# Performance work log

Measured on AMD Instinct MI355X. Metric: run time of the kernel, lower is better.

Reference implementation:

```python
import jax, jax.numpy as jnp
import numpy as np

B, S, D, NH = 8, 2048, 1024, 8
HD = D // NH          # 128 head dim
UP = 2752             # round_up(2.6667*1024, 64) gated FFN up dim
EPS = 1e-6


def setup_inputs() -> dict:
    key = jax.random.key(0)
    ks = jax.random.split(key, 10)
    s_hd = 1.0 / np.sqrt(HD)
    s_d = 1.0 / np.sqrt(D)
    s_up = 1.0 / np.sqrt(UP)
    return {
        "x": jax.random.normal(ks[0], (B, S, D), jnp.float32),
        "rms1_w": 1.0 + 0.1 * jax.random.normal(ks[1], (D,), jnp.float32),
        "rms2_w": 1.0 + 0.1 * jax.random.normal(ks[2], (D,), jnp.float32),
        # block-diagonal per-head input projections for the 4 gates (i,f,z,o)
        "Wg": jax.random.normal(ks[3], (4, NH, HD, HD), jnp.float32) * s_hd,
        # block-diagonal per-head recurrent weights for the 4 gates
        "R": jax.random.normal(ks[4], (4, NH, HD, HD), jnp.float32) * s_hd,
        "b": jax.random.normal(ks[5], (4, D), jnp.float32) * 0.1,
        "gn_w": 1.0 + 0.1 * jax.random.normal(ks[6], (D,), jnp.float32),
        "W_gate": jax.random.normal(ks[7], (D, UP), jnp.float32) * s_d,
        "W_up": jax.random.normal(ks[8], (D, UP), jnp.float32) * s_d,
        "W_down": jax.random.normal(ks[9], (UP, D), jnp.float32) * s_up,
    }


def _rmsnorm(x, w):
    xf = x.astype(jnp.float32)
    return xf * jax.lax.rsqrt(jnp.mean(xf * xf, axis=-1, keepdims=True) + EPS) * w


def _slstm_block(x, rms1_w, rms2_w, Wg, R, b, gn_w, W_gate, W_up, W_down):
    # --- norm + sLSTM layer ---
    xn = _rmsnorm(x, rms1_w)                     # [B,S,D]
    xh = xn.reshape(B, S, NH, HD)
    # precompute input-side gate preactivations for all timesteps: [S,B,4,NH,HD]
    gx = jnp.einsum('bsni,gnoi->sbgno', xh, Wg) + b.reshape(4, NH, HD)

    zeros = jnp.zeros((B, NH, HD), jnp.float32)
    init = (zeros, zeros, zeros, zeros)          # h, c, n, m

    def step(carry, g):
        h, c, n, m = carry
        pre = g + jnp.einsum('bni,gnoi->bgno', h, R)   # [B,4,NH,HD]
        ir, fr, zr, o_r = pre[:, 0], pre[:, 1], pre[:, 2], pre[:, 3]
        logfplusm = m + jax.nn.log_sigmoid(fr)
        mnew = jnp.maximum(ir, logfplusm)
        i = jnp.exp(ir - mnew)
        f = jnp.exp(logfplusm - mnew)
        cnew = f * c + i * jnp.tanh(zr)
        nnew = f * n + i
        hnew = jax.nn.sigmoid(o_r) * cnew / nnew
        return (hnew, cnew, nnew, mnew), hnew

    (hl, cl, nl, ml), hs = jax.lax.scan(step, init, gx)
    hs = jnp.transpose(hs, (1, 0, 2, 3))         # [B,S,NH,HD]
    # per-head group norm (zero-mean layernorm within each head), weight only
    mu = jnp.mean(hs, axis=-1, keepdims=True)
    var = jnp.var(hs, axis=-1, keepdims=True)
    y = ((hs - mu) * jax.lax.rsqrt(var + EPS)).reshape(B, S, D) * gn_w
    x = x + y                                    # residual
    # --- norm + gated SiLU FFN ---
    xn2 = _rmsnorm(x, rms2_w)
    ff = (jax.nn.silu(xn2 @ W_gate) * (xn2 @ W_up)) @ W_down
    out = x + ff
    state = jnp.stack([hl, cl, nl, ml])          # [4,B,NH,HD] last (h,c,n,m)
    return out, state


def reference(x, rms1_w, rms2_w, Wg, R, b, gn_w, W_gate, W_up, W_down):
    return _slstm_block(x, rms1_w, rms2_w, Wg, R, b, gn_w, W_gate, W_up, W_down)
```

## Files before the change

kernel.cpp:

```cpp
#include <hip/hip_runtime.h>

typedef __bf16 bf16;
typedef bf16 bf16x8 __attribute__((ext_vector_type(8)));
typedef bf16 bf16x4 __attribute__((ext_vector_type(4)));
typedef float f32x4 __attribute__((ext_vector_type(4)));

#define B_ 8
#define S_ 2048
#define D_ 1024
#define NH_ 8
#define HD_ 128
#define UPP 2816
#define ROWS (B_*S_)

__device__ __forceinline__ void gload_lds16(const void* gsrc, void* ldsdst) {
  __builtin_amdgcn_global_load_lds(
      (const __attribute__((address_space(1))) void*)gsrc,
      (__attribute__((address_space(3))) void*)ldsdst, 16, 0, 0);
}

__global__ __launch_bounds__(256) void pack_wgr_kernel(
    const float* __restrict__ Wg, const float* __restrict__ R, const float* __restrict__ bv,
    bf16* __restrict__ Wgpk, bf16* __restrict__ Rpk, float* __restrict__ biaspk)
{
  const float K2 = 1.442695040888963f;
  int idx = blockIdx.x * 256 + threadIdx.x;
  if (idx < 8*512*128) {
    int k = idx & 127, j = (idx >> 7) & 511, n = idx >> 16;
    int g = (j >> 4) & 3, o = ((j >> 6) << 4) | (j & 15);
    float sc = (g == 2) ? 2.f*K2 : K2;
    size_t src = (((size_t)(g*8 + n)*128 + o)*128 + k);
    Wgpk[idx] = (bf16)(Wg[src] * sc);
    Rpk[idx]  = (bf16)(R[src] * sc);
  }
  if (idx < 8*512) {
    int j = idx & 511, n = idx >> 9;
    int g = (j >> 4) & 3, o = ((j >> 6) << 4) | (j & 15);
    float sc = (g == 2) ? 2.f*K2 : K2;
    biaspk[idx] = bv[g*1024 + n*128 + o] * sc;
  }
}

__global__ __launch_bounds__(256) void packT_kernel(
    const float* __restrict__ in, bf16* __restrict__ out,
    int K_out, int N_out, int K_in, int N_in)
{
  __shared__ float tile[64][65];
  int k0 = blockIdx.x * 64, j0 = blockIdx.y * 64;
  int tj = threadIdx.x & 63, t4 = threadIdx.x >> 6;
  #pragma unroll
  for (int p = 0; p < 16; ++p) {
    int kk = p*4 + t4, k = k0 + kk, j = j0 + tj;
    tile[kk][tj] = (k < K_in && j < N_in) ? in[(size_t)k * N_in + j] : 0.f;
  }
  __syncthreads();
  #pragma unroll
  for (int p = 0; p < 16; ++p) {
    int jj = p*4 + t4, j = j0 + jj, k = k0 + tj;
    if (j < N_out && k < K_out) out[(size_t)j * K_out + k] = (bf16)tile[tj][jj];
  }
}

__global__ __launch_bounds__(256) void rmsnorm1_kernel(
    const float* __restrict__ x, const float* __restrict__ w, bf16* __restrict__ xn)
{
  const int row = blockIdx.x, t = threadIdx.x;
  const size_t base = (size_t)row * D_;
  float4 xv = ((const float4*)(x + base))[t];
  float p = xv.x*xv.x + xv.y*xv.y + xv.z*xv.z + xv.w*xv.w;
  #pragma unroll
  for (int m = 1; m <= 32; m <<= 1) p += __shfl_xor(p, m);
  __shared__ float red[4];
  if ((t & 63) == 0) red[t >> 6] = p;
  __syncthreads();
  float rs = rsqrtf((red[0]+red[1]+red[2]+red[3]) * (1.f/1024.f) + 1e-6f);
  float4 wv = ((const float4*)w)[t];
  bf16x4 o;
  o[0] = (bf16)(xv.x*rs*wv.x); o[1] = (bf16)(xv.y*rs*wv.y);
  o[2] = (bf16)(xv.z*rs*wv.z); o[3] = (bf16)(xv.w*rs*wv.w);
  ((bf16x4*)(xn + base))[t] = o;
}

#define BM 128
#define BN 128
#define BKK 64
template<int MODE>
__global__ __launch_bounds__(256) void gemm_bt(
    const bf16* __restrict__ A, int lda,
    const bf16* __restrict__ B, int ldb,
    float* Cf, bf16* Cb, int ldc,
    const float* __restrict__ bias, const float* res, const bf16* gatein, int K)
{
  __shared__ __align__(16) bf16 As[BM*BKK];
  __shared__ __align__(16) bf16 Bs[BN*BKK];
  if constexpr (MODE == 0) {
    const int h = blockIdx.z;
    A += h * HD_;
    B += (size_t)h * (512*128);
    Cb += (size_t)h * ((size_t)ROWS * 512);
    bias += h * 512;
  }
  const int tid = threadIdx.x;
  const int lane = tid & 63, wave = tid >> 6;
  const int row0 = blockIdx.y * BM, col0 = blockIdx.x * BN;
  const int srow = lane >> 3, scol = (lane & 7) * 8;
  const int wr = (wave >> 1) * 64, wc = (wave & 1) * 64;
  const int fr = lane & 15, fg = lane >> 4;
  f32x4 acc[4][4] = {};

  for (int k0 = 0; k0 < K; k0 += BKK) {
    __syncthreads();
    #pragma unroll
    for (int c = 0; c < 4; ++c) {
      const int slot = wave * 4 + c;
      const int r = slot * 8 + srow;
      gload_lds16(A + (size_t)(row0 + r) * lda + (k0 + scol), &As[slot * 512]);
      gload_lds16(B + (size_t)(col0 + r) * ldb + (k0 + scol), &Bs[slot * 512]);
    }
    __syncthreads();
    #pragma unroll
    for (int kk = 0; kk < 2; ++kk) {
      bf16x8 af[4], bfv[4];
      #pragma unroll
      for (int m = 0; m < 4; ++m)
        af[m] = *(const bf16x8*)&As[(wr + m*16 + fr)*BKK + kk*32 + fg*8];
      #pragma unroll
      for (int nn = 0; nn < 4; ++nn)
        bfv[nn] = *(const bf16x8*)&Bs[(wc + nn*16 + fr)*BKK + kk*32 + fg*8];
      #pragma unroll
      for (int m = 0; m < 4; ++m)
        #pragma unroll
        for (int nn = 0; nn < 4; ++nn)
          acc[m][nn] = __builtin_amdgcn_mfma_f32_16x16x32_bf16(af[m], bfv[nn], acc[m][nn], 0, 0, 0);
    }
  }

  #pragma unroll
  for (int m = 0; m < 4; ++m) {
    const int rbase = row0 + wr + m*16 + fg*4;
    #pragma unroll
    for (int nn = 0; nn < 4; ++nn) {
      const int col = col0 + wc + nn*16 + fr;
      #pragma unroll
      for (int j = 0; j < 4; ++j) {
        const size_t off = (size_t)(rbase + j) * ldc + col;
        float v = acc[m][nn][j];
        if constexpr (MODE == 0) Cb[off] = (bf16)(v + bias[col]);
        if constexpr (MODE == 1) Cb[off] = (bf16)v;
        if constexpr (MODE == 2) Cf[off] = v + res[off];
        if constexpr (MODE == 3) {
          float gf = (float)gatein[off];
          Cb[off] = (bf16)(gf / (1.f + __expf(-gf)) * v);
        }
      }
    }
  }
}

__global__ __launch_bounds__(256, 1) void recur_kernel(
    const bf16* __restrict__ gx, const bf16* __restrict__ Rpk,
    bf16* __restrict__ hs, float* __restrict__ stateOut)
{
  const int n = blockIdx.x;
  const int tid = threadIdx.x, w = tid >> 6, l = tid & 63;
  const int b16 = l & 15, fg = l >> 4;
  const int b8 = l & 7, q8 = (l >> 3) & 1;
  __shared__ __align__(16) bf16 H0[16*136];
  __shared__ __align__(16) bf16 H1[16*136];
  for (int i = tid; i < 16*136; i += 256) { H0[i] = (bf16)0.f; H1[i] = (bf16)0.f; }
  __syncthreads();

  bf16x8 rf[8][4];
  #pragma unroll
  for (int tt = 0; tt < 8; ++tt)
    #pragma unroll
    for (int kk = 0; kk < 4; ++kk)
      rf[tt][kk] = *(const bf16x8*)&Rpk[(size_t)n*65536 + (size_t)(w*128 + tt*16 + b16)*128 + kk*32 + fg*8];

  f32x4 zv = {0.f, 0.f, 0.f, 0.f};
  asm volatile("" : "+v"(zv));

  float cS[4] = {}, nS[4] = {}, mS[4] = {}, hv[4] = {};
  const int o0 = w*32 + q8*16 + fg*4;
  const bf16* gxp = gx + (size_t)n * ROWS * 512 + (size_t)b8 * S_ * 512
                    + (size_t)(2*w + q8) * 64 + fg*4;
  bf16* hsp = hs + (size_t)b8 * S_ * D_ + n * HD_ + o0;

  bf16x4 gb0[4], gb1[4], gb2[4], gb3[4];
  #pragma unroll
  for (int g = 0; g < 4; ++g) {
    gb0[g] = *(const bf16x4*)(gxp + (size_t)0*512 + g*16);
    gb1[g] = *(const bf16x4*)(gxp + (size_t)1*512 + g*16);
  }

  auto step = [&](bf16* Hr, bf16* Hw, int s, bf16x4 (&gU)[4], bf16x4 (&gF)[4]) {
    bf16x8 hf[4];
    #pragma unroll
    for (int kk = 0; kk < 4; ++kk)
      hf[kk] = *(const bf16x8*)&Hr[b16*136 + kk*32 + fg*8];

    {
      int sf = (s + 2 < S_) ? s + 2 : 0;
      #pragma unroll
      for (int g = 0; g < 4; ++g)
        gF[g] = *(const bf16x4*)(gxp + (size_t)sf*512 + g*16);
    }

    f32x4 acc[8];
    #pragma unroll
    for (int tt = 0; tt < 8; ++tt)
      acc[tt] = __builtin_amdgcn_mfma_f32_16x16x32_bf16(rf[tt][0], hf[0], zv, 0, 0, 0);
    #pragma unroll
    for (int kk = 1; kk < 4; ++kk)
      #pragma unroll
      for (int tt = 0; tt < 8; ++tt)
        acc[tt] = __builtin_amdgcn_mfma_f32_16x16x32_bf16(rf[tt][kk], hf[kk], acc[tt], 0, 0, 0);

    float pre[4][4];
    #pragma unroll
    for (int g = 0; g < 4; ++g)
      #pragma unroll
      for (int jj = 0; jj < 4; ++jj) {
        float other = __shfl_xor(acc[4+g][jj], 8, 64);
        pre[g][jj] = (l & 8) ? other : acc[g][jj];
      }

    #pragma unroll
    for (int jj = 0; jj < 4; ++jj) {
      float ir  = pre[0][jj] + (float)gU[0][jj];
      float fr_ = pre[1][jj] + (float)gU[1][jj];
      float zr  = pre[2][jj] + (float)gU[2][jj];
      float og  = pre[3][jj] + (float)gU[3][jj];
      float t   = __builtin_amdgcn_exp2f(-fr_);
      float lfm = mS[jj] - __builtin_amdgcn_logf(1.f + t);
      float d   = ir - lfm;
      float e   = __builtin_amdgcn_exp2f(-fabsf(d));
      float iG  = (d >= 0.f) ? 1.f : e;
      float fG  = (d >= 0.f) ? e : 1.f;
      float mn  = fmaxf(ir, lfm);
      float e2  = __builtin_amdgcn_exp2f(zr);
      float th  = 1.f - 2.f*__builtin_amdgcn_rcpf(e2 + 1.f);
      float c2  = fG*cS[jj] + iG*th;
      float n2  = fG*nS[jj] + iG;
      float eo  = __builtin_amdgcn_exp2f(-og);
      float den = n2 + n2*eo;
      cS[jj] = c2; nS[jj] = n2; mS[jj] = mn;
      hv[jj] = c2 * __builtin_amdgcn_rcpf(den);
    }

    bf16x4 hb;
    #pragma unroll
    for (int jj = 0; jj < 4; ++jj) hb[jj] = (bf16)hv[jj];
    *(bf16x4*)&Hw[b8*136 + o0] = hb;
    *(bf16x4*)(hsp + (size_t)s*D_) = hb;

    __builtin_amdgcn_sched_barrier(0);
    __builtin_amdgcn_s_waitcnt(0xC07F);
    __builtin_amdgcn_s_barrier();
    __builtin_amdgcn_sched_barrier(0);
  };

  for (int s = 0; s < S_; s += 4) {
    step(H0, H1, s,     gb0, gb2);
    step(H1, H0, s + 1, gb1, gb3);
    step(H0, H1, s + 2, gb2, gb0);
    step(H1, H0, s + 3, gb3, gb1);
  }

  {
    const float LN2 = 0.6931471805599453f;
    size_t sb = ((size_t)b8*NH_ + n)*HD_ + o0;
    *(float4*)(stateOut +         sb) = make_float4(hv[0], hv[1], hv[2], hv[3]);
    *(float4*)(stateOut +  8192 + sb) = make_float4(cS[0], cS[1], cS[2], cS[3]);
    *(float4*)(stateOut + 16384 + sb) = make_float4(nS[0], nS[1], nS[2], nS[3]);
    *(float4*)(stateOut + 24576 + sb) = make_float4(mS[0]*LN2, mS[1]*LN2, mS[2]*LN2, mS[3]*LN2);
  }
}

__global__ __launch_bounds__(256) void fuse_gn_kernel(
    const bf16* __restrict__ hs, const float* __restrict__ x,
    const float* __restrict__ gnw, const float* __restrict__ r2w,
    float* __restrict__ xr, bf16* __restrict__ xn2)
{
  const int row = blockIdx.x, t = threadIdx.x;
  const size_t base = (size_t)row * D_;
  bf16x4 hraw = ((const bf16x4*)(hs + base))[t];
  float h0 = (float)hraw[0], h1 = (float)hraw[1], h2 = (float)hraw[2], h3 = (float)hraw[3];
  float4 xv = ((const float4*)(x + base))[t];
  float sum = h0 + h1 + h2 + h3;
  float sq  = h0*h0 + h1*h1 + h2*h2 + h3*h3;
  #pragma unroll
  for (int m = 1; m <= 16; m <<= 1) { sum += __shfl_xor(sum, m); sq += __shfl_xor(sq, m); }
  float mu = sum * (1.f/128.f);
  float var = sq * (1.f/128.f) - mu*mu;
  float rstd = rsqrtf(var + 1e-6f);
  float4 gw = ((const float4*)gnw)[t];
  float r0 = xv.x + (h0-mu)*rstd*gw.x;
  float r1 = xv.y + (h1-mu)*rstd*gw.y;
  float r2 = xv.z + (h2-mu)*rstd*gw.z;
  float r3 = xv.w + (h3-mu)*rstd*gw.w;
  ((float4*)(xr + base))[t] = make_float4(r0, r1, r2, r3);
  float p = r0*r0 + r1*r1 + r2*r2 + r3*r3;
  #pragma unroll
  for (int m = 1; m <= 32; m <<= 1) p += __shfl_xor(p, m);
  __shared__ float red[4];
  if ((t & 63) == 0) red[t >> 6] = p;
  __syncthreads();
  float rs = rsqrtf((red[0]+red[1]+red[2]+red[3]) * (1.f/1024.f) + 1e-6f);
  float4 w2 = ((const float4*)r2w)[t];
  bf16x4 o;
  o[0] = (bf16)(r0*rs*w2.x); o[1] = (bf16)(r1*rs*w2.y);
  o[2] = (bf16)(r2*rs*w2.z); o[3] = (bf16)(r3*rs*w2.w);
  ((bf16x4*)(xn2 + base))[t] = o;
}

extern "C" void kernel_launch(void* const* d_in, const int* in_sizes, int n_in,
                              void* d_out, int out_size, void* d_ws, size_t ws_size,
                              hipStream_t stream)
{
  const float* x     = (const float*)d_in[0];
  const float* rms1w = (const float*)d_in[1];
  const float* rms2w = (const float*)d_in[2];
  const float* Wg    = (const float*)d_in[3];
  const float* R     = (const float*)d_in[4];
  const float* bvec  = (const float*)d_in[5];
  const float* gnw   = (const float*)d_in[6];
  const float* Wgate = (const float*)d_in[7];
  const float* Wup   = (const float*)d_in[8];
  const float* Wdown = (const float*)d_in[9];
  float* out = (float*)d_out;
  float* stateOut = out + (size_t)ROWS * D_;

  char* ws = (char*)d_ws;
  size_t off = 0;
  auto alloc = [&](size_t bytes) -> void* {
    void* p = ws + off; off += (bytes + 255) & ~(size_t)255; return p;
  };
  bf16*  xn     = (bf16*)alloc((size_t)ROWS * D_ * 2);
  bf16*  hsbuf  = (bf16*)alloc((size_t)ROWS * D_ * 2);
  bf16*  bigbuf = (bf16*)alloc((size_t)NH_ * ROWS * 512 * 2);
  bf16*  Wgpk   = (bf16*)alloc(8*512*128*2);
  bf16*  Rpk    = (bf16*)alloc(8*512*128*2);
  float* biaspk = (float*)alloc(8*512*4);
  bf16*  Wgatepk = (bf16*)alloc((size_t)UPP * D_ * 2);
  bf16*  Wuppk   = (bf16*)alloc((size_t)UPP * D_ * 2);
  bf16*  Wdownpk = (bf16*)alloc((size_t)D_ * UPP * 2);

  pack_wgr_kernel<<<2048, 256, 0, stream>>>(Wg, R, bvec, Wgpk, Rpk, biaspk);
  packT_kernel<<<dim3(16, 44), 256, 0, stream>>>(Wgate, Wgatepk, 1024, 2816, 1024, 2752);
  packT_kernel<<<dim3(16, 44), 256, 0, stream>>>(Wup,   Wuppk,   1024, 2816, 1024, 2752);
  packT_kernel<<<dim3(44, 16), 256, 0, stream>>>(Wdown, Wdownpk, 2816, 1024, 2752, 1024);

  rmsnorm1_kernel<<<ROWS, 256, 0, stream>>>(x, rms1w, xn);

  gemm_bt<0><<<dim3(4, 128, 8), 256, 0, stream>>>(xn, D_, Wgpk, 128,
      nullptr, bigbuf, 512, biaspk, nullptr, nullptr, 128);

  recur_kernel<<<8, 256, 0, stream>>>(bigbuf, Rpk, hsbuf, stateOut);

  fuse_gn_kernel<<<ROWS, 256, 0, stream>>>(hsbuf, x, gnw, rms2w, out, xn);

  bf16* gate = bigbuf;
  gemm_bt<1><<<dim3(22, 128), 256, 0, stream>>>(xn, D_, Wgatepk, D_,
      nullptr, gate, UPP, nullptr, nullptr, nullptr, D_);
  gemm_bt<3><<<dim3(22, 128), 256, 0, stream>>>(xn, D_, Wuppk, D_,
      nullptr, gate, UPP, nullptr, nullptr, gate, D_);

  gemm_bt<2><<<dim3(8, 128), 256, 0, stream>>>(gate, UPP, Wdownpk, UPP,
      out, nullptr, D_, nullptr, out, nullptr, UPP);
}
```

Before: 2.409 ms.

## Split sLSTM recurrence across batch pairs to use four times more workgroups

The recurrent kernel now launches 32 workgroups (8 heads times 4 batch pairs) instead of 8, so each block handles 2 batch rows rather than all 8. Pre-activations leave the MFMA accumulators through an LDS scratch buffer instead of lane shuffles, and each thread computes one gate output instead of four. This shortens the per-step elementwise critical path and spreads the serial scan over more compute units. In exchange each block still runs the full 16-column MFMA with mostly wasted columns, and every step adds an LDS round trip plus scalar gx loads.

```diff
diff --git a/kernel.cpp b/kernel.cpp
--- a/kernel.cpp
+++ b/kernel.cpp
@@ -161,13 +161,19 @@
     const bf16* __restrict__ gx, const bf16* __restrict__ Rpk,
     bf16* __restrict__ hs, float* __restrict__ stateOut)
 {
-  const int n = blockIdx.x;
+  const int n  = blockIdx.x >> 2;
+  const int bp = blockIdx.x & 3;
   const int tid = threadIdx.x, w = tid >> 6, l = tid & 63;
   const int b16 = l & 15, fg = l >> 4;
-  const int b8 = l & 7, q8 = (l >> 3) & 1;
-  __shared__ __align__(16) bf16 H0[16*136];
-  __shared__ __align__(16) bf16 H1[16*136];
-  for (int i = tid; i < 16*136; i += 256) { H0[i] = (bf16)0.f; H1[i] = (bf16)0.f; }
+  const int bl  = l & 1;
+  const int r   = l >> 1;
+  const int q   = r >> 4, r16 = r & 15;
+  const int b   = bp*2 + bl;
+  const int o   = w*32 + r;
+
+  __shared__ __align__(16) bf16 H[2][2][136];
+  __shared__ __align__(16) float scr[4][2][8][16];
+  for (int i = tid; i < 2*2*136; i += 256) ((bf16*)H)[i] = (bf16)0.f;
   __syncthreads();
 
   bf16x8 rf[8][4];
@@ -180,30 +186,31 @@
   f32x4 zv = {0.f, 0.f, 0.f, 0.f};
   asm volatile("" : "+v"(zv));
 
-  float cS[4] = {}, nS[4] = {}, mS[4] = {}, hv[4] = {};
-  const int o0 = w*32 + q8*16 + fg*4;
-  const bf16* gxp = gx + (size_t)n * ROWS * 512 + (size_t)b8 * S_ * 512
-                    + (size_t)(2*w + q8) * 64 + fg*4;
-  bf16* hsp = hs + (size_t)b8 * S_ * D_ + n * HD_ + o0;
-
-  bf16x4 gb0[4], gb1[4], gb2[4], gb3[4];
+  float cS = 0.f, nS = 0.f, mS = 0.f, hv = 0.f;
+
+  const bf16* gxp = gx + (size_t)n * ROWS * 512 + (size_t)b * S_ * 512
+                    + (size_t)(w*2 + q) * 64 + r16;
+  bf16* hsp = hs + (size_t)b * S_ * D_ + n * HD_ + o;
+
+  bf16 ga[4][4];
   #pragma unroll
   for (int g = 0; g < 4; ++g) {
-    gb0[g] = *(const bf16x4*)(gxp + (size_t)0*512 + g*16);
-    gb1[g] = *(const bf16x4*)(gxp + (size_t)1*512 + g*16);
-  }
-
-  auto step = [&](bf16* Hr, bf16* Hw, int s, bf16x4 (&gU)[4], bf16x4 (&gF)[4]) {
+    ga[0][g] = gxp[(size_t)0*512 + g*16];
+    ga[1][g] = gxp[(size_t)1*512 + g*16];
+  }
+
+  auto step = [&](const bf16 (&Hr)[2][136], bf16 (&Hw)[2][136], int s,
+                  bf16 (&gU)[4], bf16 (&gF)[4]) {
     bf16x8 hf[4];
     #pragma unroll
     for (int kk = 0; kk < 4; ++kk)
-      hf[kk] = *(const bf16x8*)&Hr[b16*136 + kk*32 + fg*8];
+      hf[kk] = *(const bf16x8*)&Hr[b16 & 1][kk*32 + fg*8];
 
     {
       int sf = (s + 2 < S_) ? s + 2 : 0;
       #pragma unroll
       for (int g = 0; g < 4; ++g)
-        gF[g] = *(const bf16x4*)(gxp + (size_t)sf*512 + g*16);
+        gF[g] = gxp[(size_t)sf*512 + g*16];
     }
 
     f32x4 acc[8];
@@ -216,43 +223,37 @@
       for (int tt = 0; tt < 8; ++tt)
         acc[tt] = __builtin_amdgcn_mfma_f32_16x16x32_bf16(rf[tt][kk], hf[kk], acc[tt], 0, 0, 0);
 
-    float pre[4][4];
+    if (b16 < 2) {
+      #pragma unroll
+      for (int tt = 0; tt < 8; ++tt)
+        *(f32x4*)&scr[w][b16][tt][fg*4] = acc[tt];
+    }
+    float pre[4];
     #pragma unroll
     for (int g = 0; g < 4; ++g)
-      #pragma unroll
-      for (int jj = 0; jj < 4; ++jj) {
-        float other = __shfl_xor(acc[4+g][jj], 8, 64);
-        pre[g][jj] = (l & 8) ? other : acc[g][jj];
-      }
-
-    #pragma unroll
-    for (int jj = 0; jj < 4; ++jj) {
-      float ir  = pre[0][jj] + (float)gU[0][jj];
-      float fr_ = pre[1][jj] + (float)gU[1][jj];
-      float zr  = pre[2][jj] + (float)gU[2][jj];
-      float og  = pre[3][jj] + (float)gU[3][jj];
-      float t   = __builtin_amdgcn_exp2f(-fr_);
-      float lfm = mS[jj] - __builtin_amdgcn_logf(1.f + t);
-      float d   = ir - lfm;
-      float e   = __builtin_amdgcn_exp2f(-fabsf(d));
-      float iG  = (d >= 0.f) ? 1.f : e;
-      float fG  = (d >= 0.f) ? e : 1.f;
-      float mn  = fmaxf(ir, lfm);
-      float e2  = __builtin_amdgcn_exp2f(zr);
-      float th  = 1.f - 2.f*__builtin_amdgcn_rcpf(e2 + 1.f);
-      float c2  = fG*cS[jj] + iG*th;
-      float n2  = fG*nS[jj] + iG;
-      float eo  = __builtin_amdgcn_exp2f(-og);
-      float den = n2 + n2*eo;
-      cS[jj] = c2; nS[jj] = n2; mS[jj] = mn;
-      hv[jj] = c2 * __builtin_amdgcn_rcpf(den);
-    }
-
-    bf16x4 hb;
-    #pragma unroll
-    for (int jj = 0; jj < 4; ++jj) hb[jj] = (bf16)hv[jj];
-    *(bf16x4*)&Hw[b8*136 + o0] = hb;
-    *(bf16x4*)(hsp + (size_t)s*D_) = hb;
+      pre[g] = scr[w][bl][q*4 + g][r16];
+
+    float ir  = pre[0] + (float)gU[0];
+    float fr_ = pre[1] + (float)gU[1];
+    float zr  = pre[2] + (float)gU[2];
+    float og  = pre[3] + (float)gU[3];
+    float t   = __builtin_amdgcn_exp2f(-fr_);
+    float lfm = mS - __builtin_amdgcn_logf(1.f + t);
+    float d   = ir - lfm;
+    float e   = __builtin_amdgcn_exp2f(-fabsf(d));
+    float iG  = (d >= 0.f) ? 1.f : e;
+    float fG  = (d >= 0.f) ? e : 1.f;
+    mS = fmaxf(ir, lfm);
+    float e2  = __builtin_amdgcn_exp2f(zr);
+    float th  = 1.f - 2.f*__builtin_amdgcn_rcpf(e2 + 1.f);
+    cS = fG*cS + iG*th;
+    nS = fG*nS + iG;
+    float eo  = __builtin_amdgcn_exp2f(-og);
+    hv = cS * __builtin_amdgcn_rcpf(nS + nS*eo);
+
+    bf16 hb = (bf16)hv;
+    Hw[bl][o] = hb;
+    hsp[(size_t)s*D_] = hb;
 
     __builtin_amdgcn_sched_barrier(0);
     __builtin_amdgcn_s_waitcnt(0xC07F);
@@ -261,19 +262,19 @@
   };
 
   for (int s = 0; s < S_; s += 4) {
-    step(H0, H1, s,     gb0, gb2);
-    step(H1, H0, s + 1, gb1, gb3);
-    step(H0, H1, s + 2, gb2, gb0);
-    step(H1, H0, s + 3, gb3, gb1);
+    step(H[0], H[1], s,     ga[0], ga[2]);
+    step(H[1], H[0], s + 1, ga[1], ga[3]);
+    step(H[0], H[1], s + 2, ga[2], ga[0]);
+    step(H[1], H[0], s + 3, ga[3], ga[1]);
   }
 
   {
     const float LN2 = 0.6931471805599453f;
-    size_t sb = ((size_t)b8*NH_ + n)*HD_ + o0;
-    *(float4*)(stateOut +         sb) = make_float4(hv[0], hv[1], hv[2], hv[3]);
-    *(float4*)(stateOut +  8192 + sb) = make_float4(cS[0], cS[1], cS[2], cS[3]);
-    *(float4*)(stateOut + 16384 + sb) = make_float4(nS[0], nS[1], nS[2], nS[3]);
-    *(float4*)(stateOut + 24576 + sb) = make_float4(mS[0]*LN2, mS[1]*LN2, mS[2]*LN2, mS[3]*LN2);
+    size_t sb = ((size_t)b*NH_ + n)*HD_ + o;
+    stateOut[sb]         = hv;
+    stateOut[8192  + sb] = cS;
+    stateOut[16384 + sb] = nS;
+    stateOut[24576 + sb] = mS * LN2;
   }
 }
 
@@ -356,7 +357,7 @@
   gemm_bt<0><<<dim3(4, 128, 8), 256, 0, stream>>>(xn, D_, Wgpk, 128,
       nullptr, bigbuf, 512, biaspk, nullptr, nullptr, 128);
 
-  recur_kernel<<<8, 256, 0, stream>>>(bigbuf, Rpk, hsbuf, stateOut);
+  recur_kernel<<<32, 256, 0, stream>>>(bigbuf, Rpk, hsbuf, stateOut);
 
   fuse_gn_kernel<<<ROWS, 256, 0, stream>>>(hsbuf, x, gnw, rms2w, out, xn);
 
```

Result: faster. 1.979 ms (-17.9%).
